# Optimization experiments

Hardware: AMD Instinct MI355X
Metric: run time of the kernel (lower is better)

Reference implementation:

```python
import jax, jax.numpy as jnp
import numpy as np

V, E, H, DV = 32000, 128, 512, 256
B, NV, MAXLEN = 128, 196, 32
TEMP, TOP_P = 0.8, 0.9


def setup_inputs() -> dict:
    key = jax.random.key(0)
    ks = jax.random.split(key, 22)
    def n(k, shape, s=0.02):
        return jax.random.normal(k, shape, dtype=jnp.float32) * s
    return {
        'thought': n(ks[0], (B, H), 1.0),
        'visual_features': n(ks[1], (B, NV, DV), 1.0),
        'emb': n(ks[2], (V, E)),
        'w_ih0': n(ks[3], (4 * H, E)), 'w_hh0': n(ks[4], (4 * H, H)),
        'b_ih0': n(ks[5], (4 * H,)), 'b_hh0': n(ks[6], (4 * H,)),
        'w_ih1': n(ks[7], (4 * H, H)), 'w_hh1': n(ks[8], (4 * H, H)),
        'b_ih1': n(ks[9], (4 * H,)), 'b_hh1': n(ks[10], (4 * H,)),
        'gw1': n(ks[11], (H, H)), 'gb1': n(ks[12], (H,)),
        'gw2': n(ks[13], (1, H)), 'gb2': n(ks[14], (1,)),
        'out_w': n(ks[15], (V, H)), 'out_b': n(ks[16], (V,)),
        'vis_w': n(ks[17], (H, DV)), 'vis_b': n(ks[18], (H,)),
        'ln_g': jnp.ones((H,), jnp.float32), 'ln_b': jnp.zeros((H,), jnp.float32),
        'max_len': MAXLEN,
    }


def _lstm_cell(x, h, c, wih, whh, bih, bhh):
    z = x @ wih.T + bih + h @ whh.T + bhh  # [B, 4H]
    i, f, g, o = jnp.split(z, 4, axis=-1)
    c2 = jax.nn.sigmoid(f) * c + jax.nn.sigmoid(i) * jnp.tanh(g)
    h2 = jax.nn.sigmoid(o) * jnp.tanh(c2)
    return h2, c2


def reference(thought, visual_features, emb, w_ih0, w_hh0, b_ih0, b_hh0,
              w_ih1, w_hh1, b_ih1, b_hh1, gw1, gb1, gw2, gb2,
              out_w, out_b, vis_w, vis_b, ln_g, ln_b, max_len):
    Bsz, Hd = thought.shape
    Vsz = out_w.shape[0]
    # visual projection + LayerNorm (dropout is identity at eval)
    vp = visual_features @ vis_w.T + vis_b  # [B, N, H]
    mu = vp.mean(-1, keepdims=True)
    var = vp.var(-1, keepdims=True)
    vp = (vp - mu) * jax.lax.rsqrt(var + 1e-5) * ln_g + ln_b

    key = jax.random.key(42)
    zeros = jnp.zeros_like(thought)
    tok0 = jnp.ones((Bsz,), jnp.int32)              # start token = 1
    hist0 = -jnp.ones((Bsz, 3), jnp.int32)          # last-3 token history (sentinel -1)
    carry0 = (thought, zeros, thought, zeros, tok0, hist0)
    rows = jnp.arange(Bsz)[:, None]

    def step(carry, step_idx):
        h0, c0, h1, c1, tok, hist = carry
        x = emb[tok]                                 # [B, E]
        h0, c0 = _lstm_cell(x, h0, c0, w_ih0, w_hh0, b_ih0, b_hh0)
        h1, c1 = _lstm_cell(h0, h1, c1, w_ih1, w_hh1, b_ih1, b_hh1)
        gate = jax.nn.sigmoid(jnp.tanh(h1 @ gw1.T + gb1) @ gw2.T + gb2)  # [B,1]
        o = h1 * gate
        # visual attention (single query per step)
        scores = jnp.einsum('bh,bnh->bn', o, vp) / (Hd ** 0.5)
        aw = jax.nn.softmax(scores, axis=-1)
        o = o + jnp.einsum('bn,bnh->bh', aw, vp)
        logits = o @ out_w.T + out_b                 # [B, V]
        # repetition penalty: -2.0 on each distinct token in last 3 (set semantics)
        m = jax.nn.one_hot(hist, Vsz, dtype=bool).any(axis=1)  # [B, V]
        logits = logits - 2.0 * m
        logits = logits / TEMP
        # top-p nucleus filtering
        order = jnp.argsort(-logits, axis=-1)
        sl = jnp.take_along_axis(logits, order, axis=-1)
        cum = jnp.cumsum(jax.nn.softmax(sl, axis=-1), axis=-1)
        rm = cum > TOP_P
        rm = jnp.concatenate([jnp.zeros_like(rm[:, :1]), rm[:, :-1]], axis=-1)
        rm_orig = jnp.zeros_like(rm).at[rows, order].set(rm)
        logits = jnp.where(rm_orig, -jnp.inf, logits)
        k = jax.random.fold_in(key, step_idx)
        nxt = jax.random.categorical(k, logits).astype(jnp.int32)
        hist = jnp.concatenate([hist[:, 1:], nxt[:, None]], axis=1)
        return (h0, c0, h1, c1, nxt, hist), nxt

    _, toks = jax.lax.scan(step, carry0, jnp.arange(int(max_len)))
    return toks.T  # [B, max_len]
```

## Files before the change

kernel.cpp:

```cpp
#include <hip/hip_runtime.h>
#include <stdint.h>

#define NB 128
#define NH 512
#define NE 128
#define NVOC 32000
#define NNV 196
#define NDV 256
#define NSTEPS 32
#define SORTSTRIDE 32768
#define SCHUNK 16000

static __device__ __forceinline__ uint32_t rotl32(uint32_t x, int r){
  return (x << r) | (x >> (32 - r));
}

static __device__ __forceinline__ void threefry2x32(uint32_t k0, uint32_t k1,
    uint32_t x0, uint32_t x1, uint32_t &o0, uint32_t &o1){
  uint32_t k2 = k0 ^ k1 ^ 0x1BD11BDAu;
  x0 += k0; x1 += k1;
#define TF_RND(r) { x0 += x1; x1 = rotl32(x1,(r)); x1 ^= x0; }
  TF_RND(13) TF_RND(15) TF_RND(26) TF_RND(6)
  x0 += k1; x1 += k2 + 1u;
  TF_RND(17) TF_RND(29) TF_RND(16) TF_RND(24)
  x0 += k2; x1 += k0 + 2u;
  TF_RND(13) TF_RND(15) TF_RND(26) TF_RND(6)
  x0 += k0; x1 += k1 + 3u;
  TF_RND(17) TF_RND(29) TF_RND(16) TF_RND(24)
  x0 += k1; x1 += k2 + 4u;
  TF_RND(13) TF_RND(15) TF_RND(26) TF_RND(6)
  x0 += k2; x1 += k0 + 5u;
#undef TF_RND
  o0 = x0; o1 = x1;
}

__global__ __launch_bounds__(256) void k_visproj(
    const float* __restrict__ vf, const float* __restrict__ vis_w,
    const float* __restrict__ vis_b, const float* __restrict__ ln_g,
    const float* __restrict__ ln_b, float* __restrict__ vp)
{
  int bn = blockIdx.x;
  int tid = threadIdx.x;
  __shared__ float xs[NDV];
  __shared__ float red[256];
  const float* x = vf + (size_t)bn * NDV;
  xs[tid] = x[tid];
  __syncthreads();
  float out0, out1;
  {
    const float4* h4 = (const float4*)xs;
    const float4* w0 = (const float4*)(vis_w + (size_t)tid * NDV);
    const float4* w1 = (const float4*)(vis_w + (size_t)(tid + 256) * NDV);
    float a0 = 0.f, a1 = 0.f;
    #pragma unroll 4
    for (int k = 0; k < NDV/4; k++){
      float4 hh = h4[k];
      float4 wa = w0[k], wb = w1[k];
      a0 = fmaf(hh.x, wa.x, a0); a0 = fmaf(hh.y, wa.y, a0);
      a0 = fmaf(hh.z, wa.z, a0); a0 = fmaf(hh.w, wa.w, a0);
      a1 = fmaf(hh.x, wb.x, a1); a1 = fmaf(hh.y, wb.y, a1);
      a1 = fmaf(hh.z, wb.z, a1); a1 = fmaf(hh.w, wb.w, a1);
    }
    out0 = a0 + vis_b[tid];
    out1 = a1 + vis_b[tid + 256];
  }
  red[tid] = out0 + out1; __syncthreads();
  for (int s = 128; s > 0; s >>= 1){ if (tid < s) red[tid] += red[tid + s]; __syncthreads(); }
  float mu = red[0] * (1.0f / (float)NH);
  __syncthreads();
  float d0 = out0 - mu, d1 = out1 - mu;
  red[tid] = d0*d0 + d1*d1; __syncthreads();
  for (int s = 128; s > 0; s >>= 1){ if (tid < s) red[tid] += red[tid + s]; __syncthreads(); }
  float var = red[0] * (1.0f / (float)NH);
  float r = 1.0f / sqrtf(var + 1e-5f);
  float* op = vp + (size_t)bn * NH;
  op[tid]       = d0 * r * ln_g[tid]       + ln_b[tid];
  op[tid + 256] = d1 * r * ln_g[tid + 256] + ln_b[tid + 256];
}

__global__ void k_init(const float* __restrict__ thought,
                       float* __restrict__ h0, float* __restrict__ c0,
                       float* __restrict__ h1, float* __restrict__ c1)
{
  int id = blockIdx.x * 256 + threadIdx.x;
  if (id >= NH * NB) return;
  int k = id >> 7;
  int b = id & 127;
  float v = thought[(size_t)b * NH + k];
  h0[id] = v; h1[id] = v; c0[id] = 0.f; c1[id] = 0.f;
}

template<int K1>
__global__ __launch_bounds__(256) void k_lstm(
    const float* __restrict__ wih, const float* __restrict__ whh,
    const float* __restrict__ bih, const float* __restrict__ bhh,
    const float* __restrict__ a1,
    const int*   __restrict__ toks, int step,
    const float* __restrict__ hprev, const float* __restrict__ cprev,
    float* __restrict__ hout, float* __restrict__ cout)
{
  __shared__ float As[64][64];
  __shared__ float Ws[4 * 16 * 68];
  __shared__ int tokl[64];
  int tid = threadIdx.x;
  int jl = tid & 15;
  int bg = tid >> 4;
  int jbase = blockIdx.x * 16;
  int j = jbase + jl;
  int bblk = blockIdx.y * 64;
  int bl = bg * 4;
  if (K1 == NE){
    if (tid < 64) tokl[tid] = (step == 0) ? 1 : toks[(size_t)(bblk + tid) * NSTEPS + step - 1];
  }
  __syncthreads();

  float acc[4][4];
  #pragma unroll
  for (int g = 0; g < 4; g++)
    #pragma unroll
    for (int e = 0; e < 4; e++) acc[g][e] = 0.f;

  for (int part = 0; part < 2; part++){
    const float* Wsrc = part ? whh : wih;
    const float* Asrc = part ? hprev : a1;
    const int K = part ? NH : K1;
    const bool gather = (!part) && (K1 == NE);
    for (int kc = 0; kc < K; kc += 64){
      __syncthreads();
      for (int q = tid; q < 1024; q += 256){
        int kk = q >> 4;
        int bb = (q & 15) << 2;
        float4 v;
        if (gather){
          v.x = Asrc[(size_t)tokl[bb+0] * NE + kc + kk];
          v.y = Asrc[(size_t)tokl[bb+1] * NE + kc + kk];
          v.z = Asrc[(size_t)tokl[bb+2] * NE + kc + kk];
          v.w = Asrc[(size_t)tokl[bb+3] * NE + kc + kk];
        } else {
          v = *(const float4*)(Asrc + (size_t)(kc + kk) * NB + bblk + bb);
        }
        *(float4*)&As[kk][bb] = v;
      }
      for (int q = tid; q < 1024; q += 256){
        int r = q >> 4;
        int f = q & 15;
        int g = r >> 4;
        int jj = r & 15;
        float4 w = *(const float4*)(Wsrc + (size_t)(g * NH + jbase + jj) * K + kc + f * 4);
        float* wd = &Ws[(g * 16 + jj) * 68 + f * 4];
        wd[0] = w.x; wd[1] = w.y; wd[2] = w.z; wd[3] = w.w;
      }
      __syncthreads();
      #pragma unroll 2
      for (int kk = 0; kk < 64; kk += 4){
        float4 a0 = *(const float4*)&As[kk + 0][bl];
        float4 a1v = *(const float4*)&As[kk + 1][bl];
        float4 a2 = *(const float4*)&As[kk + 2][bl];
        float4 a3 = *(const float4*)&As[kk + 3][bl];
        #pragma unroll
        for (int g = 0; g < 4; g++){
          float4 w = *(const float4*)&Ws[(g * 16 + jl) * 68 + kk];
          acc[g][0] = fmaf(a0.x, w.x, acc[g][0]);
          acc[g][1] = fmaf(a0.y, w.x, acc[g][1]);
          acc[g][2] = fmaf(a0.z, w.x, acc[g][2]);
          acc[g][3] = fmaf(a0.w, w.x, acc[g][3]);
          acc[g][0] = fmaf(a1v.x, w.y, acc[g][0]);
          acc[g][1] = fmaf(a1v.y, w.y, acc[g][1]);
          acc[g][2] = fmaf(a1v.z, w.y, acc[g][2]);
          acc[g][3] = fmaf(a1v.w, w.y, acc[g][3]);
          acc[g][0] = fmaf(a2.x, w.z, acc[g][0]);
          acc[g][1] = fmaf(a2.y, w.z, acc[g][1]);
          acc[g][2] = fmaf(a2.z, w.z, acc[g][2]);
          acc[g][3] = fmaf(a2.w, w.z, acc[g][3]);
          acc[g][0] = fmaf(a3.x, w.w, acc[g][0]);
          acc[g][1] = fmaf(a3.y, w.w, acc[g][1]);
          acc[g][2] = fmaf(a3.z, w.w, acc[g][2]);
          acc[g][3] = fmaf(a3.w, w.w, acc[g][3]);
        }
      }
    }
  }

  float bi[4];
  #pragma unroll
  for (int g = 0; g < 4; g++) bi[g] = bih[g * NH + j] + bhh[g * NH + j];
  int b0g = bblk + bl;
  float4 cp = *(const float4*)(cprev + (size_t)j * NB + b0g);
  float cpv[4] = {cp.x, cp.y, cp.z, cp.w};
  float hs[4], cs[4];
  #pragma unroll
  for (int e = 0; e < 4; e++){
    float zi = acc[0][e] + bi[0];
    float zf = acc[1][e] + bi[1];
    float zg = acc[2][e] + bi[2];
    float zo = acc[3][e] + bi[3];
    float si = 1.f / (1.f + expf(-zi));
    float sf = 1.f / (1.f + expf(-zf));
    float so = 1.f / (1.f + expf(-zo));
    float tg = tanhf(zg);
    float c2 = sf * cpv[e] + si * tg;
    cs[e] = c2;
    hs[e] = so * tanhf(c2);
  }
  *(float4*)(cout + (size_t)j * NB + b0g) = make_float4(cs[0], cs[1], cs[2], cs[3]);
  *(float4*)(hout + (size_t)j * NB + b0g) = make_float4(hs[0], hs[1], hs[2], hs[3]);
}

__global__ __launch_bounds__(256) void k_gateattn(
    const float* __restrict__ h1t,
    const float* __restrict__ gw1, const float* __restrict__ gb1,
    const float* __restrict__ gw2, const float* __restrict__ gb2,
    const float* __restrict__ vp,
    float* __restrict__ o2t)
{
  int b = blockIdx.x;
  int tid = threadIdx.x;
  __shared__ float hsm[NH];
  __shared__ float tsm[NH];
  __shared__ float osm[NH];
  __shared__ float aw[NNV];
  __shared__ float red[256];
  for (int h = tid; h < NH; h += 256) hsm[h] = h1t[(size_t)h * NB + b];
  __syncthreads();
  for (int jj = tid; jj < NH; jj += 256){
    const float4* wr = (const float4*)(gw1 + (size_t)jj * NH);
    const float4* h4 = (const float4*)hsm;
    float acc = 0.f;
    #pragma unroll 4
    for (int k = 0; k < NH/4; k++){
      float4 w = wr[k]; float4 hh = h4[k];
      acc = fmaf(hh.x, w.x, acc);
      acc = fmaf(hh.y, w.y, acc);
      acc = fmaf(hh.z, w.z, acc);
      acc = fmaf(hh.w, w.w, acc);
    }
    tsm[jj] = tanhf(acc + gb1[jj]);
  }
  __syncthreads();
  float part = 0.f;
  for (int jj = tid; jj < NH; jj += 256) part = fmaf(tsm[jj], gw2[jj], part);
  red[tid] = part; __syncthreads();
  for (int s = 128; s > 0; s >>= 1){ if (tid < s) red[tid] += red[tid + s]; __syncthreads(); }
  float gate = 1.f / (1.f + expf(-(red[0] + gb2[0])));
  __syncthreads();
  for (int h = tid; h < NH; h += 256) osm[h] = hsm[h] * gate;
  __syncthreads();
  const float* vpb = vp + (size_t)b * NNV * NH;
  float sc = 0.f;
  if (tid < NNV){
    const float4* vr = (const float4*)(vpb + (size_t)tid * NH);
    const float4* o4 = (const float4*)osm;
    float accv = 0.f;
    #pragma unroll 4
    for (int k = 0; k < NH/4; k++){
      float4 v = vr[k]; float4 oo = o4[k];
      accv = fmaf(oo.x, v.x, accv);
      accv = fmaf(oo.y, v.y, accv);
      accv = fmaf(oo.z, v.z, accv);
      accv = fmaf(oo.w, v.w, accv);
    }
    sc = accv / 22.62741699796952f;
  }
  red[tid] = (tid < NNV) ? sc : -INFINITY;
  __syncthreads();
  for (int s = 128; s > 0; s >>= 1){ if (tid < s) red[tid] = fmaxf(red[tid], red[tid + s]); __syncthreads(); }
  float mx = red[0];
  __syncthreads();
  float ev = (tid < NNV) ? expf(sc - mx) : 0.f;
  red[tid] = ev; __syncthreads();
  for (int s = 128; s > 0; s >>= 1){ if (tid < s) red[tid] += red[tid + s]; __syncthreads(); }
  float zs = red[0];
  if (tid < NNV) aw[tid] = ev / zs;
  __syncthreads();
  for (int h = tid; h < NH; h += 256){
    float accv = 0.f;
    for (int n = 0; n < NNV; n++) accv = fmaf(aw[n], vpb[(size_t)n * NH + h], accv);
    o2t[(size_t)h * NB + b] = osm[h] + accv;
  }
}

__global__ __launch_bounds__(256, 4) void k_logits(
    const float* __restrict__ o2t,
    const float* __restrict__ outw,
    const float* __restrict__ outb,
    const int* __restrict__ toks, int step,
    float* __restrict__ logits)
{
  __shared__ float osh[32][NB];
  __shared__ float wsh[32][72];
  __shared__ int hist[NB][3];
  int tid = threadIdx.x;
  int vbase = blockIdx.x * 64;
  int vl = (tid & 31) * 2;
  int b0 = (tid >> 5) * 16;
  if (tid < NB){
    hist[tid][0] = (step >= 1) ? toks[(size_t)tid * NSTEPS + step - 1] : -1;
    hist[tid][1] = (step >= 2) ? toks[(size_t)tid * NSTEPS + step - 2] : -1;
    hist[tid][2] = (step >= 3) ? toks[(size_t)tid * NSTEPS + step - 3] : -1;
  }
  float acc0[16], acc1[16];
  #pragma unroll
  for (int i = 0; i < 16; i++){ acc0[i] = 0.f; acc1[i] = 0.f; }

  for (int hc = 0; hc < NH; hc += 32){
    __syncthreads();
    #pragma unroll
    for (int q = tid; q < 1024; q += 256){
      int kk = q >> 5;
      int bb = (q & 31) << 2;
      *(float4*)&osh[kk][bb] = *(const float4*)(o2t + (size_t)(hc + kk) * NB + bb);
    }
    #pragma unroll
    for (int q = tid; q < 512; q += 256){
      int vr = q >> 3;
      int f4 = q & 7;
      float4 w = *(const float4*)(outw + (size_t)(vbase + vr) * NH + hc + f4 * 4);
      wsh[f4*4 + 0][vr] = w.x;
      wsh[f4*4 + 1][vr] = w.y;
      wsh[f4*4 + 2][vr] = w.z;
      wsh[f4*4 + 3][vr] = w.w;
    }
    __syncthreads();
    #pragma unroll 4
    for (int hl = 0; hl < 32; hl++){
      float w0 = wsh[hl][vl];
      float w1 = wsh[hl][vl + 1];
      #pragma unroll
      for (int bq = 0; bq < 4; bq++){
        float4 a = *(const float4*)&osh[hl][b0 + bq * 4];
        acc0[bq*4+0] = fmaf(a.x, w0, acc0[bq*4+0]);
        acc1[bq*4+0] = fmaf(a.x, w1, acc1[bq*4+0]);
        acc0[bq*4+1] = fmaf(a.y, w0, acc0[bq*4+1]);
        acc1[bq*4+1] = fmaf(a.y, w1, acc1[bq*4+1]);
        acc0[bq*4+2] = fmaf(a.z, w0, acc0[bq*4+2]);
        acc1[bq*4+2] = fmaf(a.z, w1, acc1[bq*4+2]);
        acc0[bq*4+3] = fmaf(a.w, w0, acc0[bq*4+3]);
        acc1[bq*4+3] = fmaf(a.w, w1, acc1[bq*4+3]);
      }
    }
  }
  __syncthreads();
  int v0 = vbase + vl;
  int v1 = v0 + 1;
  float ob0 = outb[v0], ob1 = outb[v1];
  #pragma unroll
  for (int i = 0; i < 16; i++){
    int b = b0 + i;
    float l0 = acc0[i] + ob0;
    float l1 = acc1[i] + ob1;
    int h1v = hist[b][0], h2v = hist[b][1], h3v = hist[b][2];
    if (v0 == h1v || v0 == h2v || v0 == h3v) l0 -= 2.0f;
    if (v1 == h1v || v1 == h2v || v1 == h3v) l1 -= 2.0f;
    l0 = l0 / 0.8f;
    l1 = l1 / 0.8f;
    *(float2*)(logits + (size_t)b * NVOC + v0) = make_float2(l0, l1);
  }
}

__global__ __launch_bounds__(256) void k_rowstats(
    const float* __restrict__ logits, float* __restrict__ stats)
{
  int b = blockIdx.x, tid = threadIdx.x;
  const float4* lr = (const float4*)(logits + (size_t)b * NVOC);
  float mx = -INFINITY, mn = INFINITY;
  for (int i = tid; i < NVOC/4; i += 256){
    float4 v = lr[i];
    mx = fmaxf(mx, fmaxf(fmaxf(v.x, v.y), fmaxf(v.z, v.w)));
    mn = fminf(mn, fminf(fminf(v.x, v.y), fminf(v.z, v.w)));
  }
  __shared__ float ra[256], rb[256];
  ra[tid] = mx; rb[tid] = mn; __syncthreads();
  for (int s = 128; s > 0; s >>= 1){
    if (tid < s){ ra[tid] = fmaxf(ra[tid], ra[tid+s]); rb[tid] = fminf(rb[tid], rb[tid+s]); }
    __syncthreads();
  }
  float M = ra[0], mnv = rb[0];
  __syncthreads();
  float z = 0.f;
  for (int i = tid; i < NVOC/4; i += 256){
    float4 v = lr[i];
    z += expf(v.x - M) + expf(v.y - M) + expf(v.z - M) + expf(v.w - M);
  }
  ra[tid] = z; __syncthreads();
  for (int s = 128; s > 0; s >>= 1){ if (tid < s) ra[tid] += ra[tid+s]; __syncthreads(); }
  if (tid == 0) *(float4*)(stats + b * 4) = make_float4(M, ra[0], mnv, 0.f);
}

__global__ __launch_bounds__(1024) void k_radix(
    const float* __restrict__ logits,
    float* __restrict__ sortbuf)
{
  int b = blockIdx.x, tid = threadIdx.x;
  int lane = tid & 63, w = tid >> 6;
  const float* lrow = logits + (size_t)b * NVOC;
  float* B = sortbuf + (size_t)b * SORTSTRIDE;
  __shared__ __align__(16) float row[NVOC];
  __shared__ unsigned int offs[256 * 16];
  __shared__ int wtot[16];

  int ebase = w * 2048;
  int qmax = (NVOC - ebase) >> 6;
  if (qmax > 32) qmax = 32;
  unsigned long long below = (1ull << lane) - 1ull;

  float vreg[32];
  unsigned int meta[32];

  for (int pass = 0; pass < 4; pass++){
    int sh = pass * 8;

    if (pass == 0){
      #pragma unroll
      for (int q = 0; q < 32; q++)
        if (q < qmax) vreg[q] = lrow[ebase + q * 64 + lane];
    } else {
      #pragma unroll
      for (int q = 0; q < 32; q++)
        if (q < qmax) vreg[q] = row[ebase + q * 64 + lane];
    }
    for (int i = tid; i < 4096; i += 1024) offs[i] = 0u;
    __syncthreads();

    #pragma unroll
    for (int q = 0; q < 32; q++){
      if (q < qmax){
        unsigned u = __float_as_uint(vreg[q]);
        unsigned key = ~(u ^ ((unsigned)(((int)u) >> 31) | 0x80000000u));
        unsigned d = (key >> sh) & 255u;
        unsigned long long m = ~0ull;
        #pragma unroll
        for (int bit = 0; bit < 8; bit++){
          unsigned long long bb = __ballot((d >> bit) & 1u);
          m &= ((d >> bit) & 1u) ? bb : ~bb;
        }
        int rank = __popcll(m & below);
        int cnt  = __popcll(m);
        meta[q] = d | ((unsigned)rank << 8) | ((unsigned)cnt << 14);
        if (rank == 0) offs[d * 16 + w] += (unsigned)cnt;
      }
    }
    __syncthreads();

    int fb = tid * 4;
    unsigned l0 = offs[fb], l1 = offs[fb+1], l2 = offs[fb+2], l3 = offs[fb+3];
    int v = (int)(l0 + l1 + l2 + l3);
    int inc = v;
    #pragma unroll
    for (int dd = 1; dd < 64; dd <<= 1){
      int o = __shfl_up(inc, dd);
      if (lane >= dd) inc += o;
    }
    if (lane == 63) wtot[w] = inc;
    __syncthreads();
    int woff = 0;
    #pragma unroll
    for (int ww = 0; ww < 16; ww++) woff += (ww < w) ? wtot[ww] : 0;
    unsigned run = (unsigned)(woff + inc - v);
    offs[fb]   = run; run += l0;
    offs[fb+1] = run; run += l1;
    offs[fb+2] = run; run += l2;
    offs[fb+3] = run;
    __syncthreads();

    #pragma unroll
    for (int q = 0; q < 32; q++){
      if (q < qmax){
        unsigned mt = meta[q];
        unsigned d = mt & 255u;
        int rank = (int)((mt >> 8) & 63u);
        unsigned cnt = mt >> 14;
        unsigned cur = offs[d * 16 + w];
        row[cur + rank] = vreg[q];
        if (rank == 0) offs[d * 16 + w] = cur + cnt;
      }
    }
    __syncthreads();
  }

  const float4* r4 = (const float4*)row;
  float4* b4 = (float4*)B;
  for (int i = tid; i < NVOC / 4; i += 1024) b4[i] = r4[i];
}

__global__ __launch_bounds__(1024) void k_scan(
    const float* __restrict__ sortbuf,
    const float* __restrict__ stats,
    float* __restrict__ thrv,
    int* __restrict__ thrc)
{
  int b = blockIdx.x, tid = threadIdx.x;
  const float* sbuf = sortbuf + (size_t)b * SORTSTRIDE;
  __shared__ __align__(16) float pch[SCHUNK];
  __shared__ int sh_k, sh_cross;

  float4 st4 = *(const float4*)(stats + b * 4);
  float M = st4.x, Z = st4.y;
  if (tid == 0){ sh_k = NVOC - 1; sh_cross = 0; }
  __syncthreads();

  float s = 0.f, prev = 0.f;
  uint32_t base = (uint32_t)(uintptr_t)(void*)&pch[0];

  for (int cb = 0; cb < NVOC; cb += SCHUNK){
    const float4* s4 = (const float4*)(sbuf + cb);
    for (int i = tid; i < SCHUNK/4; i += 1024){
      float4 v = s4[i];
      float4 p;
      p.x = expf(v.x - M) / Z;
      p.y = expf(v.y - M) / Z;
      p.z = expf(v.z - M) / Z;
      p.w = expf(v.w - M) / Z;
      *(float4*)&pch[i * 4] = p;
    }
    __syncthreads();

    if (tid == 0 && sh_cross == 0){
      uint32_t voff = base;
      uint32_t vend = base + SCHUNK * 4u;

#define QBLK(R0,R1,R2,R3,RQ,OFF) \
  "s_waitcnt lgkmcnt(7)\n\t" \
  "v_add_f32 %[s], %[s], " R0 "\n\t" \
  "v_add_f32 %[s], %[s], " R1 "\n\t" \
  "v_add_f32 %[s], %[s], " R2 "\n\t" \
  "v_add_f32 %[s], %[s], " R3 "\n\t" \
  "ds_read_b128 " RQ ", %[voff] offset:" OFF "\n\t"

      asm volatile(
        "s_waitcnt lgkmcnt(0)\n\t"
        "ds_read_b128 v[40:43], %[voff] offset:0\n\t"
        "ds_read_b128 v[44:47], %[voff] offset:16\n\t"
        "ds_read_b128 v[48:51], %[voff] offset:32\n\t"
        "ds_read_b128 v[52:55], %[voff] offset:48\n\t"
        "ds_read_b128 v[56:59], %[voff] offset:64\n\t"
        "ds_read_b128 v[60:63], %[voff] offset:80\n\t"
        "ds_read_b128 v[64:67], %[voff] offset:96\n\t"
        "ds_read_b128 v[68:71], %[voff] offset:112\n\t"
        "Lscan%=:\n\t"
        "v_mov_b32 %[prev], %[s]\n\t"
        QBLK("v40","v41","v42","v43","v[40:43]","128")
        QBLK("v44","v45","v46","v47","v[44:47]","144")
        QBLK("v48","v49","v50","v51","v[48:51]","160")
        QBLK("v52","v53","v54","v55","v[52:55]","176")
        QBLK("v56","v57","v58","v59","v[56:59]","192")
        QBLK("v60","v61","v62","v63","v[60:63]","208")
        QBLK("v64","v65","v66","v67","v[64:67]","224")
        QBLK("v68","v69","v70","v71","v[68:71]","240")
        "v_add_u32 %[voff], 128, %[voff]\n\t"
        "v_cmp_lt_f32 vcc, 0x3f666666, %[s]\n\t"
        "s_cbranch_vccnz Ldone%=\n\t"
        "v_cmp_lt_u32 vcc, %[voff], %[vend]\n\t"
        "s_cbranch_vccnz Lscan%=\n\t"
        "Ldone%=:\n\t"
        "s_waitcnt lgkmcnt(0)\n\t"
        : [s]"+v"(s), [voff]"+v"(voff), [prev]"+v"(prev)
        : [vend]"v"(vend)
        : "vcc", "memory",
          "v40","v41","v42","v43","v44","v45","v46","v47",
          "v48","v49","v50","v51","v52","v53","v54","v55",
          "v56","v57","v58","v59","v60","v61","v62","v63",
          "v64","v65","v66","v67","v68","v69","v70","v71");
#undef QBLK

      if (s > 0.9f){
        int il0 = (int)((voff - base) >> 2) - 32;
        float t = prev;
        int kk = 31;
        for (int q = 0; q < 32; q++){
          t = t + pch[il0 + q];
          if (t > 0.9f){ kk = q; break; }
        }
        sh_k = cb + il0 + kk;
        sh_cross = 1;
      }
    }
    __syncthreads();
    if (sh_cross) break;
  }

  if (tid == 0){
    int ks = sh_k;
    float tv = sbuf[ks];
    int jlo = ks;
    while (jlo > 0 && sbuf[jlo - 1] == tv) jlo--;
    thrv[b] = tv;
    thrc[b] = ks + 1 - jlo;
  }
}

__global__ __launch_bounds__(1024) void k_pick(
    const float* __restrict__ logits,
    const float* __restrict__ thrv,
    const int* __restrict__ thrc,
    int* __restrict__ toks,
    int step)
{
  int b = blockIdx.x, tid = threadIdx.x;
  int lane = tid & 63, w = tid >> 6;
  const float* lr = logits + (size_t)b * NVOC;
  __shared__ int wtot[16];
  __shared__ float redv[1024];
  __shared__ int redi[1024];

  float tval = thrv[b];
  int ckeep = thrc[b];

  int stt = tid * 32;
  int en = min(stt + 32, NVOC);
  int eqc = 0;
  for (int i = stt; i < en; i++) eqc += (lr[i] == tval) ? 1 : 0;
  int inc = eqc;
  #pragma unroll
  for (int dd = 1; dd < 64; dd <<= 1){
    int o = __shfl_up(inc, dd);
    if (lane >= dd) inc += o;
  }
  if (lane == 63) wtot[w] = inc;
  __syncthreads();
  int woff = 0;
  #pragma unroll
  for (int ww = 0; ww < 16; ww++) woff += (ww < w) ? wtot[ww] : 0;
  int eqrank = woff + inc - eqc;

  uint32_t fk0, fk1;
  threefry2x32(0u, 42u, 0u, (uint32_t)step, fk0, fk1);
  float best = -INFINITY;
  int besti = NVOC;
  for (int i = stt; i < en; i++){
    float l = lr[i];
    bool keep;
    if (l > tval) keep = true;
    else if (l == tval){ keep = (eqrank < ckeep); eqrank++; }
    else keep = false;
    if (keep){
      uint32_t o0, o1;
      threefry2x32(fk0, fk1, 0u, (uint32_t)(b * NVOC + i), o0, o1);
      uint32_t bits = o0 ^ o1;
      uint32_t fb = (bits >> 9) | 0x3f800000u;
      float u = __uint_as_float(fb) - 1.0f;
      if (u == 0.0f) u = 1.17549435e-38f;
      float gum = -logf(-logf(u));
      float cand = l + gum;
      if (cand > best){ best = cand; besti = i; }
    }
  }
  redv[tid] = best;
  redi[tid] = besti;
  __syncthreads();
  for (int s = 512; s > 0; s >>= 1){
    if (tid < s){
      float ov = redv[tid + s]; int oi = redi[tid + s];
      if (ov > redv[tid] || (ov == redv[tid] && oi < redi[tid])){
        redv[tid] = ov; redi[tid] = oi;
      }
    }
    __syncthreads();
  }
  if (tid == 0) toks[(size_t)b * NSTEPS + step] = redi[0];
}

extern "C" void kernel_launch(void* const* d_in, const int* in_sizes, int n_in,
                              void* d_out, int out_size, void* d_ws, size_t ws_size,
                              hipStream_t stream)
{
  (void)in_sizes; (void)n_in; (void)out_size;
  const float* thought = (const float*)d_in[0];
  const float* vfeat   = (const float*)d_in[1];
  const float* emb     = (const float*)d_in[2];
  const float* w_ih0   = (const float*)d_in[3];
  const float* w_hh0   = (const float*)d_in[4];
  const float* b_ih0   = (const float*)d_in[5];
  const float* b_hh0   = (const float*)d_in[6];
  const float* w_ih1   = (const float*)d_in[7];
  const float* w_hh1   = (const float*)d_in[8];
  const float* b_ih1   = (const float*)d_in[9];
  const float* b_hh1   = (const float*)d_in[10];
  const float* gw1     = (const float*)d_in[11];
  const float* gb1     = (const float*)d_in[12];
  const float* gw2     = (const float*)d_in[13];
  const float* gb2     = (const float*)d_in[14];
  const float* out_w   = (const float*)d_in[15];
  const float* out_b   = (const float*)d_in[16];
  const float* vis_w   = (const float*)d_in[17];
  const float* vis_b   = (const float*)d_in[18];
  const float* ln_g    = (const float*)d_in[19];
  const float* ln_b    = (const float*)d_in[20];
  int* toks = (int*)d_out;

  char* ws = (char*)d_ws;
  size_t off = 0;
  auto alloc = [&](size_t bytes) -> void* {
    void* p = ws + off;
    off += (bytes + 255) & ~(size_t)255;
    return p;
  };
  float* vp      = (float*)alloc((size_t)NB * NNV * NH * 4);
  float* h0a     = (float*)alloc((size_t)NH * NB * 4);
  float* h0b     = (float*)alloc((size_t)NH * NB * 4);
  float* c0a     = (float*)alloc((size_t)NH * NB * 4);
  float* c0b     = (float*)alloc((size_t)NH * NB * 4);
  float* h1a     = (float*)alloc((size_t)NH * NB * 4);
  float* h1b     = (float*)alloc((size_t)NH * NB * 4);
  float* c1a     = (float*)alloc((size_t)NH * NB * 4);
  float* c1b     = (float*)alloc((size_t)NH * NB * 4);
  float* o2t     = (float*)alloc((size_t)NH * NB * 4);
  float* logits  = (float*)alloc((size_t)NB * NVOC * 4);
  float* sortbuf = (float*)alloc((size_t)NB * SORTSTRIDE * 4);
  float* stats   = (float*)alloc((size_t)NB * 4 * 4);
  float* thrv    = (float*)alloc((size_t)NB * 4);
  int*   thrc    = (int*)alloc((size_t)NB * 4);
  if (off > ws_size) return;

  k_visproj<<<NB * NNV, 256, 0, stream>>>(vfeat, vis_w, vis_b, ln_g, ln_b, vp);
  k_init<<<(NH * NB + 255) / 256, 256, 0, stream>>>(thought, h0a, c0a, h1a, c1a);

  for (int step = 0; step < NSTEPS; step++){
    float *h0r, *h0w, *c0r, *c0w, *h1r, *h1w, *c1r, *c1w;
    if ((step & 1) == 0){
      h0r = h0a; h0w = h0b; c0r = c0a; c0w = c0b;
      h1r = h1a; h1w = h1b; c1r = c1a; c1w = c1b;
    } else {
      h0r = h0b; h0w = h0a; c0r = c0b; c0w = c0a;
      h1r = h1b; h1w = h1a; c1r = c1b; c1w = c1a;
    }
    k_lstm<NE><<<dim3(32, 2), 256, 0, stream>>>(
        w_ih0, w_hh0, b_ih0, b_hh0, emb, toks, step, h0r, c0r, h0w, c0w);
    k_lstm<NH><<<dim3(32, 2), 256, 0, stream>>>(
        w_ih1, w_hh1, b_ih1, b_hh1, h0w, toks, step, h1r, c1r, h1w, c1w);
    k_gateattn<<<NB, 256, 0, stream>>>(h1w, gw1, gb1, gw2, gb2, vp, o2t);
    k_logits<<<NVOC / 64, 256, 0, stream>>>(o2t, out_w, out_b, toks, step, logits);
    k_rowstats<<<NB, 256, 0, stream>>>(logits, stats);
    k_radix<<<NB, 1024, 0, stream>>>(logits, sortbuf);
    k_scan<<<NB, 1024, 0, stream>>>(sortbuf, stats, thrv, thrc);
    k_pick<<<NB, 1024, 0, stream>>>(logits, thrv, thrc, toks, step);
  }
}
```

Baseline: 21.85 ms.

## Fuse rowstats, radix sort, scan and pick into one sampling kernel

Merges the four per-step sampling kernels (row max/sum, radix sort, cumulative-probability scan, Gumbel pick) into a single block-per-row kernel. Statistics, the sorted row and the probabilities stay in shared memory, which removes three launches per step and the global round trips for stats, thresholds and the sorted-row re-read. The sorted row is still written to global memory so the threshold tie count can be read back. The cost is heavier LDS reuse (the sort buffer is overwritten with probabilities), and the max/sum phase uses only 256 of the 1024 threads.

```diff
diff --git a/kernel.cpp b/kernel.cpp
--- a/kernel.cpp
+++ b/kernel.cpp
@@ -9,7 +9,6 @@
 #define NDV 256
 #define NSTEPS 32
 #define SORTSTRIDE 32768
-#define SCHUNK 16000
 
 static __device__ __forceinline__ uint32_t rotl32(uint32_t x, int r){
   return (x << r) | (x >> (32 - r));
@@ -357,46 +356,55 @@
   }
 }
 
-__global__ __launch_bounds__(256) void k_rowstats(
-    const float* __restrict__ logits, float* __restrict__ stats)
-{
-  int b = blockIdx.x, tid = threadIdx.x;
-  const float4* lr = (const float4*)(logits + (size_t)b * NVOC);
-  float mx = -INFINITY, mn = INFINITY;
-  for (int i = tid; i < NVOC/4; i += 256){
-    float4 v = lr[i];
-    mx = fmaxf(mx, fmaxf(fmaxf(v.x, v.y), fmaxf(v.z, v.w)));
-    mn = fminf(mn, fminf(fminf(v.x, v.y), fminf(v.z, v.w)));
-  }
-  __shared__ float ra[256], rb[256];
-  ra[tid] = mx; rb[tid] = mn; __syncthreads();
-  for (int s = 128; s > 0; s >>= 1){
-    if (tid < s){ ra[tid] = fmaxf(ra[tid], ra[tid+s]); rb[tid] = fminf(rb[tid], rb[tid+s]); }
-    __syncthreads();
-  }
-  float M = ra[0], mnv = rb[0];
-  __syncthreads();
-  float z = 0.f;
-  for (int i = tid; i < NVOC/4; i += 256){
-    float4 v = lr[i];
-    z += expf(v.x - M) + expf(v.y - M) + expf(v.z - M) + expf(v.w - M);
-  }
-  ra[tid] = z; __syncthreads();
-  for (int s = 128; s > 0; s >>= 1){ if (tid < s) ra[tid] += ra[tid+s]; __syncthreads(); }
-  if (tid == 0) *(float4*)(stats + b * 4) = make_float4(M, ra[0], mnv, 0.f);
-}
-
-__global__ __launch_bounds__(1024) void k_radix(
+__global__ __launch_bounds__(1024) void k_sample(
     const float* __restrict__ logits,
-    float* __restrict__ sortbuf)
+    float* __restrict__ sortbuf,
+    int* __restrict__ toks,
+    int step)
 {
   int b = blockIdx.x, tid = threadIdx.x;
   int lane = tid & 63, w = tid >> 6;
   const float* lrow = logits + (size_t)b * NVOC;
   float* B = sortbuf + (size_t)b * SORTSTRIDE;
   __shared__ __align__(16) float row[NVOC];
-  __shared__ unsigned int offs[256 * 16];
+  __shared__ __align__(16) unsigned int offs[4096];
   __shared__ int wtot[16];
+  __shared__ float sh_tval;
+  __shared__ int sh_ckeep;
+
+  float* ra = (float*)offs;
+  if (tid < 256){
+    const float4* lr4 = (const float4*)lrow;
+    float mx = -INFINITY;
+    for (int i = tid; i < NVOC/4; i += 256){
+      float4 v = lr4[i];
+      mx = fmaxf(mx, fmaxf(fmaxf(v.x, v.y), fmaxf(v.z, v.w)));
+    }
+    ra[tid] = mx;
+  }
+  __syncthreads();
+  for (int s = 128; s > 0; s >>= 1){
+    if (tid < s) ra[tid] = fmaxf(ra[tid], ra[tid + s]);
+    __syncthreads();
+  }
+  float M = ra[0];
+  __syncthreads();
+  if (tid < 256){
+    const float4* lr4 = (const float4*)lrow;
+    float z = 0.f;
+    for (int i = tid; i < NVOC/4; i += 256){
+      float4 v = lr4[i];
+      z += expf(v.x - M) + expf(v.y - M) + expf(v.z - M) + expf(v.w - M);
+    }
+    ra[tid] = z;
+  }
+  __syncthreads();
+  for (int s = 128; s > 0; s >>= 1){
+    if (tid < s) ra[tid] += ra[tid + s];
+    __syncthreads();
+  }
+  float Z = ra[0];
+  __syncthreads();
 
   int ebase = w * 2048;
   int qmax = (NVOC - ebase) >> 6;
@@ -477,46 +485,26 @@
     __syncthreads();
   }
 
-  const float4* r4 = (const float4*)row;
-  float4* b4 = (float4*)B;
-  for (int i = tid; i < NVOC / 4; i += 1024) b4[i] = r4[i];
-}
-
-__global__ __launch_bounds__(1024) void k_scan(
-    const float* __restrict__ sortbuf,
-    const float* __restrict__ stats,
-    float* __restrict__ thrv,
-    int* __restrict__ thrc)
-{
-  int b = blockIdx.x, tid = threadIdx.x;
-  const float* sbuf = sortbuf + (size_t)b * SORTSTRIDE;
-  __shared__ __align__(16) float pch[SCHUNK];
-  __shared__ int sh_k, sh_cross;
-
-  float4 st4 = *(const float4*)(stats + b * 4);
-  float M = st4.x, Z = st4.y;
-  if (tid == 0){ sh_k = NVOC - 1; sh_cross = 0; }
-  __syncthreads();
-
-  float s = 0.f, prev = 0.f;
-  uint32_t base = (uint32_t)(uintptr_t)(void*)&pch[0];
-
-  for (int cb = 0; cb < NVOC; cb += SCHUNK){
-    const float4* s4 = (const float4*)(sbuf + cb);
-    for (int i = tid; i < SCHUNK/4; i += 1024){
-      float4 v = s4[i];
+  {
+    float4* b4 = (float4*)B;
+    for (int i = tid; i < NVOC / 4; i += 1024){
+      float4 v = *(const float4*)&row[i * 4];
+      b4[i] = v;
       float4 p;
       p.x = expf(v.x - M) / Z;
       p.y = expf(v.y - M) / Z;
       p.z = expf(v.z - M) / Z;
       p.w = expf(v.w - M) / Z;
-      *(float4*)&pch[i * 4] = p;
-    }
-    __syncthreads();
-
-    if (tid == 0 && sh_cross == 0){
-      uint32_t voff = base;
-      uint32_t vend = base + SCHUNK * 4u;
+      *(float4*)&row[i * 4] = p;
+    }
+  }
+  __syncthreads();
+
+  if (tid == 0){
+    float s = 0.f, prev = 0.f;
+    uint32_t base = (uint32_t)(uintptr_t)(void*)&row[0];
+    uint32_t voff = base;
+    uint32_t vend = base + (uint32_t)(NVOC * 4);
 
 #define QBLK(R0,R1,R2,R3,RQ,OFF) \
   "s_waitcnt lgkmcnt(7)\n\t" \
@@ -526,89 +514,70 @@
   "v_add_f32 %[s], %[s], " R3 "\n\t" \
   "ds_read_b128 " RQ ", %[voff] offset:" OFF "\n\t"
 
-      asm volatile(
-        "s_waitcnt lgkmcnt(0)\n\t"
-        "ds_read_b128 v[40:43], %[voff] offset:0\n\t"
-        "ds_read_b128 v[44:47], %[voff] offset:16\n\t"
-        "ds_read_b128 v[48:51], %[voff] offset:32\n\t"
-        "ds_read_b128 v[52:55], %[voff] offset:48\n\t"
-        "ds_read_b128 v[56:59], %[voff] offset:64\n\t"
-        "ds_read_b128 v[60:63], %[voff] offset:80\n\t"
-        "ds_read_b128 v[64:67], %[voff] offset:96\n\t"
-        "ds_read_b128 v[68:71], %[voff] offset:112\n\t"
-        "Lscan%=:\n\t"
-        "v_mov_b32 %[prev], %[s]\n\t"
-        QBLK("v40","v41","v42","v43","v[40:43]","128")
-        QBLK("v44","v45","v46","v47","v[44:47]","144")
-        QBLK("v48","v49","v50","v51","v[48:51]","160")
-        QBLK("v52","v53","v54","v55","v[52:55]","176")
-        QBLK("v56","v57","v58","v59","v[56:59]","192")
-        QBLK("v60","v61","v62","v63","v[60:63]","208")
-        QBLK("v64","v65","v66","v67","v[64:67]","224")
-        QBLK("v68","v69","v70","v71","v[68:71]","240")
-        "v_add_u32 %[voff], 128, %[voff]\n\t"
-        "v_cmp_lt_f32 vcc, 0x3f666666, %[s]\n\t"
-        "s_cbranch_vccnz Ldone%=\n\t"
-        "v_cmp_lt_u32 vcc, %[voff], %[vend]\n\t"
-        "s_cbranch_vccnz Lscan%=\n\t"
-        "Ldone%=:\n\t"
-        "s_waitcnt lgkmcnt(0)\n\t"
-        : [s]"+v"(s), [voff]"+v"(voff), [prev]"+v"(prev)
-        : [vend]"v"(vend)
-        : "vcc", "memory",
-          "v40","v41","v42","v43","v44","v45","v46","v47",
-          "v48","v49","v50","v51","v52","v53","v54","v55",
-          "v56","v57","v58","v59","v60","v61","v62","v63",
-          "v64","v65","v66","v67","v68","v69","v70","v71");
+    asm volatile(
+      "s_waitcnt lgkmcnt(0)\n\t"
+      "ds_read_b128 v[40:43], %[voff] offset:0\n\t"
+      "ds_read_b128 v[44:47], %[voff] offset:16\n\t"
+      "ds_read_b128 v[48:51], %[voff] offset:32\n\t"
+      "ds_read_b128 v[52:55], %[voff] offset:48\n\t"
+      "ds_read_b128 v[56:59], %[voff] offset:64\n\t"
+      "ds_read_b128 v[60:63], %[voff] offset:80\n\t"
+      "ds_read_b128 v[64:67], %[voff] offset:96\n\t"
+      "ds_read_b128 v[68:71], %[voff] offset:112\n\t"
+      "Lscan%=:\n\t"
+      "v_mov_b32 %[prev], %[s]\n\t"
+      QBLK("v40","v41","v42","v43","v[40:43]","128")
+      QBLK("v44","v45","v46","v47","v[44:47]","144")
+      QBLK("v48","v49","v50","v51","v[48:51]","160")
+      QBLK("v52","v53","v54","v55","v[52:55]","176")
+      QBLK("v56","v57","v58","v59","v[56:59]","192")
+      QBLK("v60","v61","v62","v63","v[60:63]","208")
+      QBLK("v64","v65","v66","v67","v[64:67]","224")
+      QBLK("v68","v69","v70","v71","v[68:71]","240")
+      "v_add_u32 %[voff], 128, %[voff]\n\t"
+      "v_cmp_lt_f32 vcc, 0x3f666666, %[s]\n\t"
+      "s_cbranch_vccnz Ldone%=\n\t"
+      "v_cmp_lt_u32 vcc, %[voff], %[vend]\n\t"
+      "s_cbranch_vccnz Lscan%=\n\t"
+      "Ldone%=:\n\t"
+      "s_waitcnt lgkmcnt(0)\n\t"
+      : [s]"+v"(s), [voff]"+v"(voff), [prev]"+v"(prev)
+      : [vend]"v"(vend)
+      : "vcc", "memory",
+        "v40","v41","v42","v43","v44","v45","v46","v47",
+        "v48","v49","v50","v51","v52","v53","v54","v55",
+        "v56","v57","v58","v59","v60","v61","v62","v63",
+        "v64","v65","v66","v67","v68","v69","v70","v71");
 #undef QBLK
 
-      if (s > 0.9f){
-        int il0 = (int)((voff - base) >> 2) - 32;
-        float t = prev;
-        int kk = 31;
-        for (int q = 0; q < 32; q++){
-          t = t + pch[il0 + q];
-          if (t > 0.9f){ kk = q; break; }
-        }
-        sh_k = cb + il0 + kk;
-        sh_cross = 1;
+    int ks = NVOC - 1;
+    if (s > 0.9f){
+      int il0 = (int)((voff - base) >> 2) - 32;
+      float t = prev;
+      int kk = 31;
+      for (int q = 0; q < 32; q++){
+        t = t + row[il0 + q];
+        if (t > 0.9f){ kk = q; break; }
       }
-    }
-    __syncthreads();
-    if (sh_cross) break;
-  }
-
-  if (tid == 0){
-    int ks = sh_k;
-    float tv = sbuf[ks];
+      ks = il0 + kk;
+    }
+    float tv = B[ks];
     int jlo = ks;
-    while (jlo > 0 && sbuf[jlo - 1] == tv) jlo--;
-    thrv[b] = tv;
-    thrc[b] = ks + 1 - jlo;
-  }
-}
-
-__global__ __launch_bounds__(1024) void k_pick(
-    const float* __restrict__ logits,
-    const float* __restrict__ thrv,
-    const int* __restrict__ thrc,
-    int* __restrict__ toks,
-    int step)
-{
-  int b = blockIdx.x, tid = threadIdx.x;
-  int lane = tid & 63, w = tid >> 6;
-  const float* lr = logits + (size_t)b * NVOC;
-  __shared__ int wtot[16];
-  __shared__ float redv[1024];
-  __shared__ int redi[1024];
-
-  float tval = thrv[b];
-  int ckeep = thrc[b];
+    while (jlo > 0 && B[jlo - 1] == tv) jlo--;
+    sh_tval = tv;
+    sh_ckeep = ks + 1 - jlo;
+  }
+  __syncthreads();
+
+  float tval = sh_tval;
+  int ckeep = sh_ckeep;
+  float* redv = (float*)offs;
+  int*   redi = (int*)(offs + 1024);
 
   int stt = tid * 32;
   int en = min(stt + 32, NVOC);
   int eqc = 0;
-  for (int i = stt; i < en; i++) eqc += (lr[i] == tval) ? 1 : 0;
+  for (int i = stt; i < en; i++) eqc += (lrow[i] == tval) ? 1 : 0;
   int inc = eqc;
   #pragma unroll
   for (int dd = 1; dd < 64; dd <<= 1){
@@ -627,7 +596,7 @@
   float best = -INFINITY;
   int besti = NVOC;
   for (int i = stt; i < en; i++){
-    float l = lr[i];
+    float l = lrow[i];
     bool keep;
     if (l > tval) keep = true;
     else if (l == tval){ keep = (eqrank < ckeep); eqrank++; }
@@ -636,8 +605,8 @@
       uint32_t o0, o1;
       threefry2x32(fk0, fk1, 0u, (uint32_t)(b * NVOC + i), o0, o1);
       uint32_t bits = o0 ^ o1;
-      uint32_t fb = (bits >> 9) | 0x3f800000u;
-      float u = __uint_as_float(fb) - 1.0f;
+      uint32_t fb2 = (bits >> 9) | 0x3f800000u;
+      float u = __uint_as_float(fb2) - 1.0f;
       if (u == 0.0f) u = 1.17549435e-38f;
       float gum = -logf(-logf(u));
       float cand = l + gum;
@@ -706,9 +675,6 @@
   float* o2t     = (float*)alloc((size_t)NH * NB * 4);
   float* logits  = (float*)alloc((size_t)NB * NVOC * 4);
   float* sortbuf = (float*)alloc((size_t)NB * SORTSTRIDE * 4);
-  float* stats   = (float*)alloc((size_t)NB * 4 * 4);
-  float* thrv    = (float*)alloc((size_t)NB * 4);
-  int*   thrc    = (int*)alloc((size_t)NB * 4);
   if (off > ws_size) return;
 
   k_visproj<<<NB * NNV, 256, 0, stream>>>(vfeat, vis_w, vis_b, ln_g, ln_b, vp);
@@ -729,9 +695,6 @@
         w_ih1, w_hh1, b_ih1, b_hh1, h0w, toks, step, h1r, c1r, h1w, c1w);
     k_gateattn<<<NB, 256, 0, stream>>>(h1w, gw1, gb1, gw2, gb2, vp, o2t);
     k_logits<<<NVOC / 64, 256, 0, stream>>>(o2t, out_w, out_b, toks, step, logits);
-    k_rowstats<<<NB, 256, 0, stream>>>(logits, stats);
-    k_radix<<<NB, 1024, 0, stream>>>(logits, sortbuf);
-    k_scan<<<NB, 1024, 0, stream>>>(sortbuf, stats, thrv, thrc);
-    k_pick<<<NB, 1024, 0, stream>>>(logits, thrv, thrc, toks, step);
-  }
-}
+    k_sample<<<NB, 1024, 0, stream>>>(logits, sortbuf, toks, step);
+  }
+}
```

New measurement: 21.41 ms. 2.0% less time.
